# Optimization experiments

Measured on AMD Instinct MI355X. Metric: run time of the kernel, lower is better.

The kernel has to match this reference:

```python
import jax, jax.numpy as jnp
import numpy as np

B = 2_000_000
ND = 3

def _skew(v):
    # v: [B,3] -> [B,3,3] skew-symmetric matrix
    z = jnp.zeros_like(v[..., 0])
    r0 = jnp.stack([z, -v[..., 2], v[..., 1]], axis=-1)
    r1 = jnp.stack([v[..., 2], z, -v[..., 0]], axis=-1)
    r2 = jnp.stack([-v[..., 1], v[..., 0], z], axis=-1)
    return jnp.stack([r0, r1, r2], axis=-2)

def _rotmat(v):
    # Closed-form expm of skew(v) (Rodrigues). Mathematically identical to tf.linalg.expm.
    th2 = jnp.sum(v * v, axis=-1)                      # [B]
    th = jnp.sqrt(th2)
    small = th < 1e-6
    th_s = jnp.where(small, 1.0, th)
    th2_s = jnp.where(small, 1.0, th2)
    a = jnp.where(small, 1.0, jnp.sin(th) / th_s)      # sin(t)/t
    b = jnp.where(small, 0.5, (1.0 - jnp.cos(th)) / th2_s)  # (1-cos t)/t^2
    K = _skew(v)                                       # [B,3,3]
    I = jnp.eye(ND, dtype=v.dtype)
    return I + a[:, None, None] * K + b[:, None, None] * jnp.matmul(K, K)

def setup_inputs() -> dict:
    key = jax.random.key(0)
    k1, k2, k3, k4 = jax.random.split(key, 4)
    trans = jax.random.normal(k1, (B, ND), dtype=jnp.float32)
    rotat = jax.random.normal(k2, (B, ND), dtype=jnp.float32)
    scal_dir = jax.random.normal(k3, (B, ND), dtype=jnp.float32)
    scal = jax.random.normal(k4, (B, ND), dtype=jnp.float32)
    return {"trans": trans, "rotat": rotat, "scal_dir": scal_dir, "scal": scal}

def reference(trans, rotat, scal_dir, scal):
    R = _rotmat(rotat)          # [B,3,3] rotation
    U = _rotmat(scal_dir)       # [B,3,3] scaling direction
    D = jnp.exp(scal)           # expm(diag(s)) == diag(exp(s)), [B,3]
    # U @ diag(D) @ U^T, then R @ (.)
    Ut = jnp.swapaxes(U, -1, -2)
    M = jnp.matmul(U, D[:, :, None] * Ut)   # diag(D) @ U^T broadcast as row-scaling
    M = jnp.matmul(R, M)
    return jnp.concatenate([M, trans[:, :, None]], axis=2)  # [B,3,4]
```

## Files before the change

### kernel.cpp

```cpp
#include <hip/hip_runtime.h>
#include <math.h>

#define TPB 256

__device__ __forceinline__ void rodrigues(float v0, float v1, float v2, float R[9]) {
    float th2 = v0 * v0 + v1 * v1 + v2 * v2;
    float th  = sqrtf(th2);
    float s, c;
    sincosf(th, &s, &c);
    bool  sm = th < 1e-6f;
    float a  = sm ? 1.0f : s / th;
    float b  = sm ? 0.5f : (1.0f - c) / th2;
    float cc = 1.0f - b * th2;
    R[0] = cc + b * v0 * v0;      R[1] = b * v0 * v1 - a * v2;  R[2] = b * v0 * v2 + a * v1;
    R[3] = b * v0 * v1 + a * v2;  R[4] = cc + b * v1 * v1;      R[5] = b * v1 * v2 - a * v0;
    R[6] = b * v0 * v2 - a * v1;  R[7] = b * v1 * v2 + a * v0;  R[8] = cc + b * v2 * v2;
}

__global__ __launch_bounds__(TPB) void aff_kernel(
    const float4* __restrict__ trans,
    const float4* __restrict__ rotat,
    const float4* __restrict__ sdir,
    const float4* __restrict__ scal,
    float4* __restrict__ out,
    int B)
{
    __shared__ float s_in[4][TPB * 3];
    __shared__ float s_out[TPB * 12];

    const int tid  = threadIdx.x;
    const int base = blockIdx.x * TPB;
    const int n    = min(TPB, B - base);
    const int nf4  = (n * 3) >> 2;

    if (tid < nf4) {
        const int gbase = (base * 3) >> 2;
        float4 a = trans[gbase + tid];
        float4 b = rotat[gbase + tid];
        float4 c = sdir [gbase + tid];
        float4 d = scal [gbase + tid];
        ((float4*)&s_in[0][0])[tid] = a;
        ((float4*)&s_in[1][0])[tid] = b;
        ((float4*)&s_in[2][0])[tid] = c;
        ((float4*)&s_in[3][0])[tid] = d;
    }
    __syncthreads();

    if (tid < n) {
        float t0 = s_in[0][3*tid+0], t1 = s_in[0][3*tid+1], t2 = s_in[0][3*tid+2];

        float R[9], U[9];
        rodrigues(s_in[1][3*tid+0], s_in[1][3*tid+1], s_in[1][3*tid+2], R);
        rodrigues(s_in[2][3*tid+0], s_in[2][3*tid+1], s_in[2][3*tid+2], U);
        float d0 = expf(s_in[3][3*tid+0]);
        float d1 = expf(s_in[3][3*tid+1]);
        float d2 = expf(s_in[3][3*tid+2]);

        float W[9];
#pragma unroll
        for (int i = 0; i < 3; ++i) {
            W[3*i+0] = U[3*i+0] * d0;
            W[3*i+1] = U[3*i+1] * d1;
            W[3*i+2] = U[3*i+2] * d2;
        }
        float S[9];
#pragma unroll
        for (int i = 0; i < 3; ++i)
#pragma unroll
            for (int j = 0; j < 3; ++j)
                S[3*i+j] = W[3*i+0]*U[3*j+0] + W[3*i+1]*U[3*j+1] + W[3*i+2]*U[3*j+2];
        float M[9];
#pragma unroll
        for (int i = 0; i < 3; ++i)
#pragma unroll
            for (int j = 0; j < 3; ++j)
                M[3*i+j] = R[3*i+0]*S[0+j] + R[3*i+1]*S[3+j] + R[3*i+2]*S[6+j];

        float4* so = (float4*)s_out;
        so[3*tid+0] = make_float4(M[0], M[1], M[2], t0);
        so[3*tid+1] = make_float4(M[3], M[4], M[5], t1);
        so[3*tid+2] = make_float4(M[6], M[7], M[8], t2);
    }
    __syncthreads();

    const int nq = n * 3;
    const float4* so = (const float4*)s_out;
    const int ob = base * 3;
#pragma unroll
    for (int p = 0; p < 3; ++p) {
        int idx = p * TPB + tid;
        if (idx < nq) out[ob + idx] = so[idx];
    }
}

extern "C" void kernel_launch(void* const* d_in, const int* in_sizes, int n_in,
                              void* d_out, int out_size, void* d_ws, size_t ws_size,
                              hipStream_t stream) {
    const float4* tr = (const float4*)d_in[0];
    const float4* ro = (const float4*)d_in[1];
    const float4* sd = (const float4*)d_in[2];
    const float4* sc = (const float4*)d_in[3];
    float4* out = (float4*)d_out;

    int B = in_sizes[0] / 3;
    int blocks = (B + TPB - 1) / TPB;
    aff_kernel<<<blocks, TPB, 0, stream>>>(tr, ro, sd, sc, out, B);
}
```

Measured before the change: 175.6 us.

## Process four elements per thread with direct float4 loads, drop shared staging

```diff
diff --git a/kernel.cpp b/kernel.cpp
--- a/kernel.cpp
+++ b/kernel.cpp
@@ -17,7 +17,45 @@
     R[6] = b * v0 * v2 - a * v1;  R[7] = b * v1 * v2 + a * v0;  R[8] = cc + b * v2 * v2;
 }
 
-__global__ __launch_bounds__(TPB) void aff_kernel(
+__device__ __forceinline__ void affine_one(
+    float r0, float r1, float r2,
+    float u0, float u1, float u2,
+    float s0, float s1, float s2,
+    float t0, float t1, float t2,
+    float4* __restrict__ o)
+{
+    float R[9], U[9];
+    rodrigues(r0, r1, r2, R);
+    rodrigues(u0, u1, u2, U);
+    float d0 = expf(s0), d1 = expf(s1), d2 = expf(s2);
+
+    float W0 = U[0]*d0, W1 = U[1]*d1, W2 = U[2]*d2;
+    float W3 = U[3]*d0, W4 = U[4]*d1, W5 = U[5]*d2;
+    float W6 = U[6]*d0, W7 = U[7]*d1, W8 = U[8]*d2;
+
+    float S00 = W0*U[0] + W1*U[1] + W2*U[2];
+    float S01 = W0*U[3] + W1*U[4] + W2*U[5];
+    float S02 = W0*U[6] + W1*U[7] + W2*U[8];
+    float S11 = W3*U[3] + W4*U[4] + W5*U[5];
+    float S12 = W3*U[6] + W4*U[7] + W5*U[8];
+    float S22 = W6*U[6] + W7*U[7] + W8*U[8];
+
+    float M00 = R[0]*S00 + R[1]*S01 + R[2]*S02;
+    float M01 = R[0]*S01 + R[1]*S11 + R[2]*S12;
+    float M02 = R[0]*S02 + R[1]*S12 + R[2]*S22;
+    float M10 = R[3]*S00 + R[4]*S01 + R[5]*S02;
+    float M11 = R[3]*S01 + R[4]*S11 + R[5]*S12;
+    float M12 = R[3]*S02 + R[4]*S12 + R[5]*S22;
+    float M20 = R[6]*S00 + R[7]*S01 + R[8]*S02;
+    float M21 = R[6]*S01 + R[7]*S11 + R[8]*S12;
+    float M22 = R[6]*S02 + R[7]*S12 + R[8]*S22;
+
+    o[0] = make_float4(M00, M01, M02, t0);
+    o[1] = make_float4(M10, M11, M12, t1);
+    o[2] = make_float4(M20, M21, M22, t2);
+}
+
+__global__ __launch_bounds__(TPB, 4) void aff_kernel(
     const float4* __restrict__ trans,
     const float4* __restrict__ rotat,
     const float4* __restrict__ sdir,
@@ -25,84 +63,43 @@
     float4* __restrict__ out,
     int B)
 {
-    __shared__ float s_in[4][TPB * 3];
-    __shared__ float s_out[TPB * 12];
+    const int nfull = B >> 2;
+    const int g = blockIdx.x * TPB + threadIdx.x;
 
-    const int tid  = threadIdx.x;
-    const int base = blockIdx.x * TPB;
-    const int n    = min(TPB, B - base);
-    const int nf4  = (n * 3) >> 2;
+    if (g < nfull) {
+        const int ib = 3 * g;
+        float4 ta = trans[ib], tb = trans[ib+1], tc = trans[ib+2];
+        float4 ra = rotat[ib], rb = rotat[ib+1], rc = rotat[ib+2];
+        float4 ua = sdir [ib], ub = sdir [ib+1], uc = sdir [ib+2];
+        float4 sa = scal [ib], sb = scal [ib+1], sc = scal [ib+2];
 
-    if (tid < nf4) {
-        const int gbase = (base * 3) >> 2;
-        float4 a = trans[gbase + tid];
-        float4 b = rotat[gbase + tid];
-        float4 c = sdir [gbase + tid];
-        float4 d = scal [gbase + tid];
-        ((float4*)&s_in[0][0])[tid] = a;
-        ((float4*)&s_in[1][0])[tid] = b;
-        ((float4*)&s_in[2][0])[tid] = c;
-        ((float4*)&s_in[3][0])[tid] = d;
-    }
-    __syncthreads();
-
-    if (tid < n) {
-        float t0 = s_in[0][3*tid+0], t1 = s_in[0][3*tid+1], t2 = s_in[0][3*tid+2];
-
-        float R[9], U[9];
-        rodrigues(s_in[1][3*tid+0], s_in[1][3*tid+1], s_in[1][3*tid+2], R);
-        rodrigues(s_in[2][3*tid+0], s_in[2][3*tid+1], s_in[2][3*tid+2], U);
-        float d0 = expf(s_in[3][3*tid+0]);
-        float d1 = expf(s_in[3][3*tid+1]);
-        float d2 = expf(s_in[3][3*tid+2]);
-
-        float W[9];
-#pragma unroll
-        for (int i = 0; i < 3; ++i) {
-            W[3*i+0] = U[3*i+0] * d0;
-            W[3*i+1] = U[3*i+1] * d1;
-            W[3*i+2] = U[3*i+2] * d2;
+        float4* o = out + 12 * g;
+        affine_one(ra.x,ra.y,ra.z, ua.x,ua.y,ua.z, sa.x,sa.y,sa.z, ta.x,ta.y,ta.z, o);
+        affine_one(ra.w,rb.x,rb.y, ua.w,ub.x,ub.y, sa.w,sb.x,sb.y, ta.w,tb.x,tb.y, o+3);
+        affine_one(rb.z,rb.w,rc.x, ub.z,ub.w,uc.x, sb.z,sb.w,sc.x, tb.z,tb.w,tc.x, o+6);
+        affine_one(rc.y,rc.z,rc.w, uc.y,uc.z,uc.w, sc.y,sc.z,sc.w, tc.y,tc.z,tc.w, o+9);
+    } else if (g == nfull && (B & 3)) {
+        const float* tf = (const float*)trans;
+        const float* rf = (const float*)rotat;
+        const float* uf = (const float*)sdir;
+        const float* sf = (const float*)scal;
+        for (int e = 4 * nfull; e < B; ++e) {
+            affine_one(rf[3*e],rf[3*e+1],rf[3*e+2],
+                       uf[3*e],uf[3*e+1],uf[3*e+2],
+                       sf[3*e],sf[3*e+1],sf[3*e+2],
+                       tf[3*e],tf[3*e+1],tf[3*e+2],
+                       out + 3*e);
         }
-        float S[9];
-#pragma unroll
-        for (int i = 0; i < 3; ++i)
-#pragma unroll
-            for (int j = 0; j < 3; ++j)
-                S[3*i+j] = W[3*i+0]*U[3*j+0] + W[3*i+1]*U[3*j+1] + W[3*i+2]*U[3*j+2];
-        float M[9];
-#pragma unroll
-        for (int i = 0; i < 3; ++i)
-#pragma unroll
-            for (int j = 0; j < 3; ++j)
-                M[3*i+j] = R[3*i+0]*S[0+j] + R[3*i+1]*S[3+j] + R[3*i+2]*S[6+j];
-
-        float4* so = (float4*)s_out;
-        so[3*tid+0] = make_float4(M[0], M[1], M[2], t0);
-        so[3*tid+1] = make_float4(M[3], M[4], M[5], t1);
-        so[3*tid+2] = make_float4(M[6], M[7], M[8], t2);
-    }
-    __syncthreads();
-
-    const int nq = n * 3;
-    const float4* so = (const float4*)s_out;
-    const int ob = base * 3;
-#pragma unroll
-    for (int p = 0; p < 3; ++p) {
-        int idx = p * TPB + tid;
-        if (idx < nq) out[ob + idx] = so[idx];
     }
 }
 
 extern "C" void kernel_launch(void* const* d_in, const int* in_sizes, int n_in,
                               void* d_out, int out_size, void* d_ws, size_t ws_size,
                               hipStream_t stream) {
-    const float4* tr = (const float4*)d_in[0];
-    const float4* ro = (const float4*)d_in[1];
-    const float4* sd = (const float4*)d_in[2];
-    const float4* sc = (const float4*)d_in[3];
-    float4* out = (float4*)d_out;
-
     int B = in_sizes[0] / 3;
-    int blocks = (B + TPB - 1) / TPB;
-    aff_kernel<<<blocks, TPB, 0, stream>>>(tr, ro, sd, sc, out, B);
+    int groups = (B >> 2) + ((B & 3) ? 1 : 0);
+    int blocks = (groups + TPB - 1) / TPB;
+    aff_kernel<<<blocks, TPB, 0, stream>>>((const float4*)d_in[0], (const float4*)d_in[1],
+                                           (const float4*)d_in[2], (const float4*)d_in[3],
+                                           (float4*)d_out, B);
 }
```

Result: slower. 202.5 us (+15.3%).

## Process multiple tiles per block with register prefetch of the next tile

Applied to the files above, without the earlier changes.

```diff
diff --git a/kernel.cpp b/kernel.cpp
--- a/kernel.cpp
+++ b/kernel.cpp
@@ -2,6 +2,7 @@
 #include <math.h>
 
 #define TPB 256
+#define NT  4
 
 __device__ __forceinline__ void rodrigues(float v0, float v1, float v2, float R[9]) {
     float th2 = v0 * v0 + v1 * v1 + v2 * v2;
@@ -23,86 +24,109 @@
     const float4* __restrict__ sdir,
     const float4* __restrict__ scal,
     float4* __restrict__ out,
-    int B)
+    int B, int T)
 {
-    __shared__ float s_in[4][TPB * 3];
-    __shared__ float s_out[TPB * 12];
+    __shared__ float4 s_in [TPB * 3];
+    __shared__ float4 s_out[TPB * 3];
 
-    const int tid  = threadIdx.x;
-    const int base = blockIdx.x * TPB;
-    const int n    = min(TPB, B - base);
-    const int nf4  = (n * 3) >> 2;
+    const int tid = threadIdx.x;
 
-    if (tid < nf4) {
-        const int gbase = (base * 3) >> 2;
-        float4 a = trans[gbase + tid];
-        float4 b = rotat[gbase + tid];
-        float4 c = sdir [gbase + tid];
-        float4 d = scal [gbase + tid];
-        ((float4*)&s_in[0][0])[tid] = a;
-        ((float4*)&s_in[1][0])[tid] = b;
-        ((float4*)&s_in[2][0])[tid] = c;
-        ((float4*)&s_in[3][0])[tid] = d;
+    const float4* p0 = (tid < 192) ? (trans + tid)        : (rotat + (tid - 192));
+    const float4* p1 = (tid < 128) ? (rotat + (tid + 64)) : (sdir  + (tid - 128));
+    const float4* p2 = (tid < 64)  ? (sdir + (tid + 128)) : (scal  + (tid - 64));
+    const int o0 = (tid < 192) ? tid       : tid - 192;
+    const int o1 = (tid < 128) ? tid + 64  : tid - 128;
+    const int o2 = (tid < 64)  ? tid + 128 : tid - 64;
+
+    int tile = blockIdx.x * NT;
+    if (tile >= T) return;
+    const int tend = (tile + NT < T) ? tile + NT : T;
+
+    float4 r0 = make_float4(0.f, 0.f, 0.f, 0.f);
+    float4 r1 = r0, r2 = r0;
+
+    {
+        const int gb  = tile * (TPB * 3 / 4);
+        const int n   = min(TPB, B - tile * TPB);
+        const int nq4 = (n * 3) >> 2;
+        if (o0 < nq4) r0 = p0[gb];
+        if (o1 < nq4) r1 = p1[gb];
+        if (o2 < nq4) r2 = p2[gb];
     }
-    __syncthreads();
 
-    if (tid < n) {
-        float t0 = s_in[0][3*tid+0], t1 = s_in[0][3*tid+1], t2 = s_in[0][3*tid+2];
+    for (; tile < tend; ++tile) {
+        const int base = tile * TPB;
+        const int n    = min(TPB, B - base);
 
-        float R[9], U[9];
-        rodrigues(s_in[1][3*tid+0], s_in[1][3*tid+1], s_in[1][3*tid+2], R);
-        rodrigues(s_in[2][3*tid+0], s_in[2][3*tid+1], s_in[2][3*tid+2], U);
-        float d0 = expf(s_in[3][3*tid+0]);
-        float d1 = expf(s_in[3][3*tid+1]);
-        float d2 = expf(s_in[3][3*tid+2]);
+        s_in[tid]       = r0;
+        s_in[tid + 256] = r1;
+        s_in[tid + 512] = r2;
+        __syncthreads();
 
-        float W[9];
+        if (tile + 1 < tend) {
+            const int gb  = (tile + 1) * (TPB * 3 / 4);
+            const int n2  = min(TPB, B - (tile + 1) * TPB);
+            const int nq4 = (n2 * 3) >> 2;
+            if (o0 < nq4) r0 = p0[gb];
+            if (o1 < nq4) r1 = p1[gb];
+            if (o2 < nq4) r2 = p2[gb];
+        }
+
+        if (tid < n) {
+            const float* sf = (const float*)s_in;
+            const float t0 = sf[3*tid+0], t1 = sf[3*tid+1], t2 = sf[3*tid+2];
+
+            float R[9], U[9];
+            rodrigues(sf[ 768+3*tid+0], sf[ 768+3*tid+1], sf[ 768+3*tid+2], R);
+            rodrigues(sf[1536+3*tid+0], sf[1536+3*tid+1], sf[1536+3*tid+2], U);
+            const float d0 = expf(sf[2304+3*tid+0]);
+            const float d1 = expf(sf[2304+3*tid+1]);
+            const float d2 = expf(sf[2304+3*tid+2]);
+
+            const float W0 = U[0]*d0, W1 = U[1]*d1, W2 = U[2]*d2;
+            const float W3 = U[3]*d0, W4 = U[4]*d1, W5 = U[5]*d2;
+            const float W6 = U[6]*d0, W7 = U[7]*d1, W8 = U[8]*d2;
+
+            const float S00 = W0*U[0] + W1*U[1] + W2*U[2];
+            const float S01 = W0*U[3] + W1*U[4] + W2*U[5];
+            const float S02 = W0*U[6] + W1*U[7] + W2*U[8];
+            const float S11 = W3*U[3] + W4*U[4] + W5*U[5];
+            const float S12 = W3*U[6] + W4*U[7] + W5*U[8];
+            const float S22 = W6*U[6] + W7*U[7] + W8*U[8];
+
+            const float M00 = R[0]*S00 + R[1]*S01 + R[2]*S02;
+            const float M01 = R[0]*S01 + R[1]*S11 + R[2]*S12;
+            const float M02 = R[0]*S02 + R[1]*S12 + R[2]*S22;
+            const float M10 = R[3]*S00 + R[4]*S01 + R[5]*S02;
+            const float M11 = R[3]*S01 + R[4]*S11 + R[5]*S12;
+            const float M12 = R[3]*S02 + R[4]*S12 + R[5]*S22;
+            const float M20 = R[6]*S00 + R[7]*S01 + R[8]*S02;
+            const float M21 = R[6]*S01 + R[7]*S11 + R[8]*S12;
+            const float M22 = R[6]*S02 + R[7]*S12 + R[8]*S22;
+
+            s_out[3*tid+0] = make_float4(M00, M01, M02, t0);
+            s_out[3*tid+1] = make_float4(M10, M11, M12, t1);
+            s_out[3*tid+2] = make_float4(M20, M21, M22, t2);
+        }
+        __syncthreads();
+
+        const int nq = n * 3;
+        const int ob = base * 3;
 #pragma unroll
-        for (int i = 0; i < 3; ++i) {
-            W[3*i+0] = U[3*i+0] * d0;
-            W[3*i+1] = U[3*i+1] * d1;
-            W[3*i+2] = U[3*i+2] * d2;
+        for (int p = 0; p < 3; ++p) {
+            const int idx = p * TPB + tid;
+            if (idx < nq) out[ob + idx] = s_out[idx];
         }
-        float S[9];
-#pragma unroll
-        for (int i = 0; i < 3; ++i)
-#pragma unroll
-            for (int j = 0; j < 3; ++j)
-                S[3*i+j] = W[3*i+0]*U[3*j+0] + W[3*i+1]*U[3*j+1] + W[3*i+2]*U[3*j+2];
-        float M[9];
-#pragma unroll
-        for (int i = 0; i < 3; ++i)
-#pragma unroll
-            for (int j = 0; j < 3; ++j)
-                M[3*i+j] = R[3*i+0]*S[0+j] + R[3*i+1]*S[3+j] + R[3*i+2]*S[6+j];
-
-        float4* so = (float4*)s_out;
-        so[3*tid+0] = make_float4(M[0], M[1], M[2], t0);
-        so[3*tid+1] = make_float4(M[3], M[4], M[5], t1);
-        so[3*tid+2] = make_float4(M[6], M[7], M[8], t2);
-    }
-    __syncthreads();
-
-    const int nq = n * 3;
-    const float4* so = (const float4*)s_out;
-    const int ob = base * 3;
-#pragma unroll
-    for (int p = 0; p < 3; ++p) {
-        int idx = p * TPB + tid;
-        if (idx < nq) out[ob + idx] = so[idx];
     }
 }
 
 extern "C" void kernel_launch(void* const* d_in, const int* in_sizes, int n_in,
                               void* d_out, int out_size, void* d_ws, size_t ws_size,
                               hipStream_t stream) {
-    const float4* tr = (const float4*)d_in[0];
-    const float4* ro = (const float4*)d_in[1];
-    const float4* sd = (const float4*)d_in[2];
-    const float4* sc = (const float4*)d_in[3];
-    float4* out = (float4*)d_out;
-
     int B = in_sizes[0] / 3;
-    int blocks = (B + TPB - 1) / TPB;
-    aff_kernel<<<blocks, TPB, 0, stream>>>(tr, ro, sd, sc, out, B);
+    int T = (B + TPB - 1) / TPB;
+    int blocks = (T + NT - 1) / NT;
+    aff_kernel<<<blocks, TPB, 0, stream>>>((const float4*)d_in[0], (const float4*)d_in[1],
+                                           (const float4*)d_in[2], (const float4*)d_in[3],
+                                           (float4*)d_out, B, T);
 }
```

After: 180.7 us. 1.03x slower.
